# Kernel tuning notes

Hardware: AMD Instinct MI355X
Metric: run time of the kernel (lower is better)

The kernel has to match this reference:

```python
import jax, jax.numpy as jnp
import numpy as np

D_MODEL = 1024
N_HEADS = 16
HEAD_D = D_MODEL // N_HEADS  # 64


def setup_inputs() -> dict:
    key = jax.random.key(0)
    ks = jax.random.split(key, 10)
    s = 1.0 / np.sqrt(D_MODEL)
    x = jax.random.normal(ks[0], (4, 2048, D_MODEL), dtype=jnp.float32)
    # Per-head Q/K/V linears stacked along a head axis: W [H, d_model, d], b [H, d]
    Wq = jax.random.uniform(ks[1], (N_HEADS, D_MODEL, HEAD_D), jnp.float32, -s, s)
    bq = jax.random.uniform(ks[2], (N_HEADS, HEAD_D), jnp.float32, -s, s)
    Wk = jax.random.uniform(ks[3], (N_HEADS, D_MODEL, HEAD_D), jnp.float32, -s, s)
    bk = jax.random.uniform(ks[4], (N_HEADS, HEAD_D), jnp.float32, -s, s)
    Wv = jax.random.uniform(ks[5], (N_HEADS, D_MODEL, HEAD_D), jnp.float32, -s, s)
    bv = jax.random.uniform(ks[6], (N_HEADS, HEAD_D), jnp.float32, -s, s)
    Wo = jax.random.uniform(ks[7], (D_MODEL, D_MODEL), jnp.float32, -s, s)
    bo = jax.random.uniform(ks[8], (D_MODEL,), jnp.float32, -s, s)
    return {"x": x, "Wq": Wq, "bq": bq, "Wk": Wk, "bk": bk,
            "Wv": Wv, "bv": bv, "Wo": Wo, "bo": bo}


def reference(x, Wq, bq, Wk, bk, Wv, bv, Wo, bo):
    # x: [B, S, M]; per-head projections -> [B, H, S, d]
    Q = jnp.einsum('bsm,hmd->bhsd', x, Wq) + bq[None, :, None, :]
    K = jnp.einsum('bsm,hmd->bhsd', x, Wk) + bk[None, :, None, :]
    V = jnp.einsum('bsm,hmd->bhsd', x, Wv) + bv[None, :, None, :]
    scale = 1.0 / jnp.sqrt(jnp.asarray(HEAD_D, dtype=x.dtype))
    scores = jnp.einsum('bhqd,bhkd->bhqk', Q, K) * scale  # [B, H, S, S]
    attn = jax.nn.softmax(scores, axis=-1)
    out = jnp.einsum('bhqk,bhkd->bhqd', attn, V)  # [B, H, S, d]
    B, H, S, d = out.shape
    out = out.transpose(0, 2, 1, 3).reshape(B, S, H * d)  # concat heads
    # final projection (dropout is identity in eval mode)
    return out @ Wo.T + bo
```

## Files before the change

### kernel.cpp

```cpp
#include <hip/hip_runtime.h>
#include <stdint.h>

#define DEVI __device__ __forceinline__

typedef float f32x4 __attribute__((ext_vector_type(4)));
typedef float f32x16 __attribute__((ext_vector_type(16)));
typedef float float4v __attribute__((ext_vector_type(4)));
typedef short short8 __attribute__((ext_vector_type(8)));
typedef uint16_t u16x4 __attribute__((ext_vector_type(4)));
typedef uint32_t u32x4 __attribute__((ext_vector_type(4)));
typedef int i32x2 __attribute__((ext_vector_type(2)));

static constexpr float QSCALE = 0.125f * 1.44269504088896340736f;

DEVI uint16_t f2bf(float f) {
  uint32_t u = __builtin_bit_cast(uint32_t, f);
  return (uint16_t)((u + 0x7FFFu + ((u >> 16) & 1u)) >> 16);
}

DEVI void gload_lds16(const void* g, void* lds) {
  __builtin_amdgcn_global_load_lds(
      reinterpret_cast<const uint32_t __attribute__((address_space(1)))*>(
          reinterpret_cast<uintptr_t>(g)),
      reinterpret_cast<uint32_t __attribute__((address_space(3)))*>(
          reinterpret_cast<uintptr_t>(lds)),
      16, 0, 0);
}

DEVI short8 lds_frag(const uint16_t* tile, int row, int kByte) {
  return *(const short8*)((const char*)tile + row * 128 + (kByte ^ ((row & 7) << 4)));
}

DEVI f32x4 mfma16(short8 a, short8 b, f32x4 c) {
  return __builtin_amdgcn_mfma_f32_16x16x32_bf16(a, b, c, 0, 0, 0);
}
DEVI f32x16 mfma32(short8 a, short8 b, f32x16 c) {
  return __builtin_amdgcn_mfma_f32_32x32x16_bf16(a, b, c, 0, 0, 0);
}

DEVI uint32_t cvtpk(float lo, float hi) {
  uint32_t r;
  asm("v_cvt_pk_bf16_f32 %0, %1, %2" : "=v"(r) : "v"(lo), "v"(hi));
  return r;
}


__global__ void k_cvt_x(const float* __restrict__ x, uint16_t* __restrict__ xb) {
  const int i = blockIdx.x * blockDim.x + threadIdx.x;
  const float4v* p = (const float4v*)x + (size_t)i * 2;
  float4v a = p[0], b = p[1];
  alignas(16) uint16_t r[8];
  r[0] = f2bf(a[0]); r[1] = f2bf(a[1]); r[2] = f2bf(a[2]); r[3] = f2bf(a[3]);
  r[4] = f2bf(b[0]); r[5] = f2bf(b[1]); r[6] = f2bf(b[2]); r[7] = f2bf(b[3]);
  *((short8*)xb + i) = *(const short8*)r;
}

__global__ void k_cvt_wo(const float* __restrict__ Wo, uint16_t* __restrict__ Wob) {
  const int i = blockIdx.x * blockDim.x + threadIdx.x;
  const float4v* p = (const float4v*)Wo + (size_t)i * 2;
  float4v a = p[0], b = p[1];
  alignas(16) uint16_t r[8];
  r[0] = f2bf(a[0]); r[1] = f2bf(a[1]); r[2] = f2bf(a[2]); r[3] = f2bf(a[3]);
  r[4] = f2bf(b[0]); r[5] = f2bf(b[1]); r[6] = f2bf(b[2]); r[7] = f2bf(b[3]);
  *((short8*)Wob + i) = *(const short8*)r;
}

__global__ void k_cvt_wqkv(const float* __restrict__ Wq, const float* __restrict__ Wk,
                           const float* __restrict__ Wv, uint16_t* __restrict__ Wt) {
  __shared__ float tile[64][65];
  const int bx = blockIdx.x;
  const int sect = bx >> 8, h = (bx >> 4) & 15, kc = bx & 15;
  const float* W = sect == 0 ? Wq : (sect == 1 ? Wk : Wv);
  const float scal = sect == 0 ? QSCALE : 1.0f;
  const int t = threadIdx.x;
  const int r = t >> 2, cbase = (t & 3) * 16;
  const float* src = W + ((size_t)(h * 1024 + kc * 64 + r)) * 64 + cbase;
#pragma unroll
  for (int j = 0; j < 4; ++j) {
    float4v v = *(const float4v*)(src + j * 4);
    tile[r][cbase + j * 4 + 0] = v[0];
    tile[r][cbase + j * 4 + 1] = v[1];
    tile[r][cbase + j * 4 + 2] = v[2];
    tile[r][cbase + j * 4 + 3] = v[3];
  }
  __syncthreads();
  const int dd = t >> 2, kp = (t & 3) * 16;
  alignas(16) uint16_t tmp[16];
#pragma unroll
  for (int j = 0; j < 16; ++j) tmp[j] = f2bf(tile[kp + j][dd] * scal);
  const int n = sect * 1024 + h * 64 + dd;
  uint16_t* dst = Wt + (size_t)n * 1024 + kc * 64 + kp;
  *(short8*)dst = *(const short8*)tmp;
  *((short8*)dst + 1) = *(const short8*)(tmp + 8);
}

template <int MODE>
__global__ __launch_bounds__(256, 2) void gemm_k1024(
    const uint16_t* __restrict__ A, const uint16_t* __restrict__ Bt, int tiles_n,
    const float* __restrict__ bias_q, const float* __restrict__ bias_k,
    const float* __restrict__ bias_v,
    uint16_t* __restrict__ Qws, uint16_t* __restrict__ Kws, uint16_t* __restrict__ Vtws,
    float* __restrict__ outf) {
  __shared__ uint16_t As[2][128 * 64];
  __shared__ uint16_t Bs[2][128 * 64];

  const int tid = threadIdx.x, lane = tid & 63, wv = tid >> 6;
  const int m0 = (blockIdx.x / tiles_n) * 128;
  const int n0 = (blockIdx.x % tiles_n) * 128;
  const int wm = (wv >> 1) * 64, wn = (wv & 1) * 64;
  const int rin = lane >> 3;
  const int csw = ((lane & 7) ^ rin) * 16;

  const char* gA = (const char*)A;
  const char* gB = (const char*)Bt;

  f32x4 acc[4][4];
#pragma unroll
  for (int mi = 0; mi < 4; ++mi)
#pragma unroll
    for (int ni = 0; ni < 4; ++ni) acc[mi][ni] = (f32x4){0.f, 0.f, 0.f, 0.f};

  auto stage = [&](int buf, int kt) {
    const int k0b = kt * 128;
#pragma unroll
    for (int i = 0; i < 4; ++i) {
      const int rb = wv * 32 + i * 8;
      gload_lds16(gA + (size_t)(m0 + rb + rin) * 2048 + k0b + csw, &As[buf][rb * 64]);
      gload_lds16(gB + (size_t)(n0 + rb + rin) * 2048 + k0b + csw, &Bs[buf][rb * 64]);
    }
  };

  stage(0, 0);
  const int kb0 = (lane >> 4) * 16;
  for (int kt = 0; kt < 16; ++kt) {
    const int buf = kt & 1;
    __syncthreads();
    if (kt + 1 < 16) stage(buf ^ 1, kt + 1);
#pragma unroll
    for (int kk = 0; kk < 2; ++kk) {
      short8 af[4], bfr[4];
#pragma unroll
      for (int i = 0; i < 4; ++i) {
        af[i] = lds_frag(As[buf], wm + i * 16 + (lane & 15), kk * 64 + kb0);
        bfr[i] = lds_frag(Bs[buf], wn + i * 16 + (lane & 15), kk * 64 + kb0);
      }
#pragma unroll
      for (int mi = 0; mi < 4; ++mi)
#pragma unroll
        for (int ni = 0; ni < 4; ++ni) acc[mi][ni] = mfma16(af[mi], bfr[ni], acc[mi][ni]);
    }
  }

  const int col0 = n0 + wn + (lane & 15);
  const int row0 = m0 + wm + ((lane >> 4) << 2);
  if (MODE == 1) {
#pragma unroll
    for (int ni = 0; ni < 4; ++ni) {
      const int n = col0 + ni * 16;
      const float bv = bias_q[n];
#pragma unroll
      for (int mi = 0; mi < 4; ++mi) {
        const int mrow = row0 + mi * 16;
#pragma unroll
        for (int r = 0; r < 4; ++r)
          outf[(size_t)(mrow + r) * 1024 + n] = acc[mi][ni][r] + bv;
      }
    }
  } else {
#pragma unroll
    for (int ni = 0; ni < 4; ++ni) {
      const int n = col0 + ni * 16;
      const int sect = n >> 10, h = (n >> 6) & 15, dd = n & 63;
      float bv;
      if (sect == 0) bv = bias_q[h * 64 + dd] * QSCALE;
      else if (sect == 1) bv = bias_k[h * 64 + dd];
      else bv = bias_v[h * 64 + dd];
#pragma unroll
      for (int mi = 0; mi < 4; ++mi) {
        const int mrow = row0 + mi * 16;
        const int b = mrow >> 11, s = mrow & 2047;
        const int bh = b * 16 + h;
        if (sect == 2) {
          u16x4 pk;
#pragma unroll
          for (int r = 0; r < 4; ++r) pk[r] = f2bf(acc[mi][ni][r] + bv);
          *(u16x4*)(Vtws + ((size_t)bh * 64 + dd) * 2048 + s) = pk;
        } else {
          uint16_t* dst = (sect == 0 ? Qws : Kws) + ((size_t)bh * 2048 + s) * 64 + dd;
#pragma unroll
          for (int r = 0; r < 4; ++r) dst[(size_t)r * 64] = f2bf(acc[mi][ni][r] + bv);
        }
      }
    }
  }
}

__global__ __launch_bounds__(256, 2) void attn_fa(
    const uint16_t* __restrict__ Qws, const uint16_t* __restrict__ Kws,
    const uint16_t* __restrict__ Vtws, uint16_t* __restrict__ AttO) {
  __shared__ uint16_t Kl[2][64 * 64];
  __shared__ uint16_t Vl[2][64 * 64];

  const int tid = threadIdx.x, lane = tid & 63, wq = tid >> 6;
  const int bid = blockIdx.x;
  const int bh = (bid & 7) * 8 + (bid >> 7);
  const int q0 = ((bid >> 3) & 15) * 128;
  const int hi = lane >> 5;
  const int qc = lane & 31;

  const uint16_t* Qb = Qws + (size_t)bh * (2048 * 64);
  const uint16_t* Kb = Kws + (size_t)bh * (2048 * 64);
  const uint16_t* Vb = Vtws + (size_t)bh * (64 * 2048);

  const int lrow = lane >> 3;
  const int csw = ((lane & 7) ^ lrow) * 16;

  short8 qf[4];
  const int qrow = q0 + wq * 32 + qc;
#pragma unroll
  for (int c = 0; c < 4; ++c)
    qf[c] = *(const short8*)(Qb + (size_t)qrow * 64 + c * 16 + hi * 8);

  short8 ones;
#pragma unroll
  for (int j = 0; j < 8; ++j) ones[j] = (short)0x3F80;

  f32x16 o0 = {}, o1 = {};
  f32x16 accL = {};
  float m = 8.0f;

  auto stage = [&](int buf, int kt) {
    const int kv0 = kt * 64;
#pragma unroll
    for (int i = 0; i < 2; ++i) {
      const int rb = i * 32 + wq * 8;
      const int rt = rb + lrow;
      gload_lds16((const char*)Kb + (size_t)(kv0 + rt) * 128 + csw,
                  (char*)&Kl[buf][0] + rb * 128);
      gload_lds16((const char*)Vb + ((size_t)rt * 2048 + kv0) * 2 + csw,
                  (char*)&Vl[buf][0] + rb * 128);
    }
  };

  stage(0, 0);
  for (int kt = 0; kt < 32; ++kt) {
    const int buf = kt & 1;
    __syncthreads();
    if (kt + 1 < 32) stage(buf ^ 1, kt + 1);

    f32x16 p0 = {}, p1 = {};
    __builtin_amdgcn_s_setprio(1);
#pragma unroll
    for (int c = 0; c < 4; ++c) {
      short8 k0 = lds_frag(&Kl[buf][0], qc, c * 32 + hi * 16);
      short8 k1 = lds_frag(&Kl[buf][0], 32 + qc, c * 32 + hi * 16);
      p0 = mfma32(k0, qf[c], p0);
      p1 = mfma32(k1, qf[c], p1);
    }
    __builtin_amdgcn_s_setprio(0);

    float t8[8];
#pragma unroll
    for (int r = 0; r < 8; ++r)
      t8[r] = fmaxf(fmaxf(p0[2 * r], p0[2 * r + 1]),
                    fmaxf(p1[2 * r], p1[2 * r + 1]));
#pragma unroll
    for (int r = 0; r < 4; ++r) t8[r] = fmaxf(t8[r], t8[r + 4]);
    float mx = fmaxf(fmaxf(t8[0], t8[1]), fmaxf(t8[2], t8[3]));
    mx = fmaxf(mx, __shfl_xor(mx, 32, 64));
    if (__any(mx - m > 8.0f)) {
      const float nm = fmaxf(m, mx);
      const float al = __builtin_amdgcn_exp2f(m - nm);
      accL[0] *= al;
#pragma unroll
      for (int r = 0; r < 16; ++r) { o0[r] *= al; o1[r] *= al; }
      m = nm;
    }
#pragma unroll
    for (int r = 0; r < 16; ++r) p0[r] = __builtin_amdgcn_exp2f(p0[r] - m);
#pragma unroll
    for (int r = 0; r < 16; ++r) p1[r] = __builtin_amdgcn_exp2f(p1[r] - m);

    short8 pa[4];
#pragma unroll
    for (int km = 0; km < 2; ++km) {
#pragma unroll
      for (int bb = 0; bb < 2; ++bb) {
        const f32x16& p = km ? p1 : p0;
        uint32_t X0 = cvtpk(p[8 * bb + 0], p[8 * bb + 1]);
        uint32_t Y0 = cvtpk(p[8 * bb + 4], p[8 * bb + 5]);
        uint32_t X1 = cvtpk(p[8 * bb + 2], p[8 * bb + 3]);
        uint32_t Y1 = cvtpk(p[8 * bb + 6], p[8 * bb + 7]);
        i32x2 s0 = __builtin_amdgcn_permlane32_swap((int)X0, (int)Y0, false, false);
        i32x2 s1 = __builtin_amdgcn_permlane32_swap((int)X1, (int)Y1, false, false);
        u32x4 dw = {(uint32_t)s0[0], (uint32_t)s1[0], (uint32_t)s0[1], (uint32_t)s1[1]};
        pa[km * 2 + bb] = __builtin_bit_cast(short8, dw);
      }
    }

    __builtin_amdgcn_s_setprio(1);
#pragma unroll
    for (int ks = 0; ks < 4; ++ks) {
      short8 v0 = lds_frag(&Vl[buf][0], qc, ks * 32 + hi * 16);
      short8 v1 = lds_frag(&Vl[buf][0], 32 + qc, ks * 32 + hi * 16);
      o0 = mfma32(v0, pa[ks], o0);
      o1 = mfma32(v1, pa[ks], o1);
      accL = mfma32(ones, pa[ks], accL);
    }
    __builtin_amdgcn_s_setprio(0);
  }
  __syncthreads();

  const float inv = 1.0f / accL[0];
#pragma unroll
  for (int r = 0; r < 16; ++r) { o0[r] *= inv; o1[r] *= inv; }

  uint16_t* ep = (uint16_t*)Kl + wq * 2048;
#pragma unroll
  for (int no = 0; no < 2; ++no)
#pragma unroll
    for (int rg = 0; rg < 4; ++rg) {
      const f32x16& oo = no ? o1 : o0;
      const int d0 = no * 32 + rg * 8 + hi * 4;
      u16x4 pk;
#pragma unroll
      for (int j = 0; j < 4; ++j) pk[j] = f2bf(oo[rg * 4 + j]);
      *(u16x4*)((char*)ep + qc * 128 + ((d0 * 2) ^ ((qc & 7) << 4))) = pk;
    }
  const int b = bh >> 4, h = bh & 15;
#pragma unroll
  for (int it = 0; it < 4; ++it) {
    const int pos = it * 64 + lane;
    const int qq = pos >> 3, c = pos & 7;
    short8 vv = *(const short8*)((const char*)ep + qq * 128 + ((c * 16) ^ ((qq & 7) << 4)));
    *(short8*)(AttO + ((size_t)b * 2048 + q0 + wq * 32 + qq) * 1024 + h * 64 + c * 8) = vv;
  }
}


extern "C" void kernel_launch(void* const* d_in, const int* in_sizes, int n_in,
                              void* d_out, int out_size, void* d_ws, size_t ws_size,
                              hipStream_t stream) {
  (void)in_sizes; (void)n_in; (void)out_size; (void)ws_size;
  const float* x  = (const float*)d_in[0];
  const float* Wq = (const float*)d_in[1];
  const float* bq = (const float*)d_in[2];
  const float* Wk = (const float*)d_in[3];
  const float* bk = (const float*)d_in[4];
  const float* Wv = (const float*)d_in[5];
  const float* bv = (const float*)d_in[6];
  const float* Wo = (const float*)d_in[7];
  const float* bo = (const float*)d_in[8];
  float* out = (float*)d_out;

  char* ws = (char*)d_ws;
  uint16_t* Xb   = (uint16_t*)(ws);
  uint16_t* AttO = (uint16_t*)(ws);
  uint16_t* Wqkv = (uint16_t*)(ws + 16777216);
  uint16_t* Wob  = (uint16_t*)(ws + 23068672);
  uint16_t* Qws  = (uint16_t*)(ws + 25165824);
  uint16_t* Kws  = (uint16_t*)(ws + 41943040);
  uint16_t* Vt   = (uint16_t*)(ws + 58720256);

  k_cvt_x<<<4096, 256, 0, stream>>>(x, Xb);
  k_cvt_wqkv<<<768, 256, 0, stream>>>(Wq, Wk, Wv, Wqkv);
  k_cvt_wo<<<512, 256, 0, stream>>>(Wo, Wob);
  gemm_k1024<0><<<64 * 24, 256, 0, stream>>>(Xb, Wqkv, 24, bq, bk, bv, Qws, Kws, Vt, nullptr);
  attn_fa<<<1024, 256, 0, stream>>>(Qws, Kws, Vt, AttO);
  gemm_k1024<1><<<64 * 8, 256, 0, stream>>>(AttO, Wob, 8, bo, nullptr, nullptr,
                                            nullptr, nullptr, nullptr, out);
}
```

Measured before the change: 199.1 us.

## Process two query groups per wave in attention, compute row sums on VALU, swizzle GEMM blocks

Each attention wave now handles 64 query rows as two 32-row groups that share the same K/V LDS fragments. This halves the grid to 512 blocks and doubles K/V reuse per load. The softmax denominator is now a VALU sum with a cross-half shuffle instead of an extra MFMA against a ones vector. The GEMM kernels also remap block IDs with an XCD-style swizzle to improve L2 locality. In exchange, register pressure rises from the doubled accumulators, and with fewer blocks occupancy and wave-level parallelism may drop.

```diff
diff --git a/kernel.cpp b/kernel.cpp
--- a/kernel.cpp
+++ b/kernel.cpp
@@ -42,6 +42,35 @@
   uint32_t r;
   asm("v_cvt_pk_bf16_f32 %0, %1, %2" : "=v"(r) : "v"(lo), "v"(hi));
   return r;
+}
+
+DEVI void mk_pa(const f32x16& p0, const f32x16& p1, short8* pa) {
+#pragma unroll
+  for (int km = 0; km < 2; ++km) {
+#pragma unroll
+    for (int bb = 0; bb < 2; ++bb) {
+      const f32x16& p = km ? p1 : p0;
+      uint32_t X0 = cvtpk(p[8 * bb + 0], p[8 * bb + 1]);
+      uint32_t Y0 = cvtpk(p[8 * bb + 4], p[8 * bb + 5]);
+      uint32_t X1 = cvtpk(p[8 * bb + 2], p[8 * bb + 3]);
+      uint32_t Y1 = cvtpk(p[8 * bb + 6], p[8 * bb + 7]);
+      i32x2 s0 = __builtin_amdgcn_permlane32_swap((int)X0, (int)Y0, false, false);
+      i32x2 s1 = __builtin_amdgcn_permlane32_swap((int)X1, (int)Y1, false, false);
+      u32x4 dw = {(uint32_t)s0[0], (uint32_t)s1[0], (uint32_t)s0[1], (uint32_t)s1[1]};
+      pa[km * 2 + bb] = __builtin_bit_cast(short8, dw);
+    }
+  }
+}
+
+DEVI float tree_max(const f32x16& p0, const f32x16& p1) {
+  float t8[8];
+#pragma unroll
+  for (int r = 0; r < 8; ++r)
+    t8[r] = fmaxf(fmaxf(p0[2 * r], p0[2 * r + 1]),
+                  fmaxf(p1[2 * r], p1[2 * r + 1]));
+#pragma unroll
+  for (int r = 0; r < 4; ++r) t8[r] = fmaxf(t8[r], t8[r + 4]);
+  return fmaxf(fmaxf(t8[0], t8[1]), fmaxf(t8[2], t8[3]));
 }
 
 
@@ -105,8 +134,11 @@
   __shared__ uint16_t Bs[2][128 * 64];
 
   const int tid = threadIdx.x, lane = tid & 63, wv = tid >> 6;
-  const int m0 = (blockIdx.x / tiles_n) * 128;
-  const int n0 = (blockIdx.x % tiles_n) * 128;
+  const int cpx = (MODE == 0) ? 192 : 64;
+  const int bid = blockIdx.x;
+  const int swz = (bid & 7) * cpx + (bid >> 3);
+  const int m0 = (swz / tiles_n) * 128;
+  const int n0 = (swz % tiles_n) * 128;
   const int wm = (wv >> 1) * 64, wn = (wv & 1) * 64;
   const int rin = lane >> 3;
   const int csw = ((lane & 7) ^ rin) * 16;
@@ -198,13 +230,12 @@
 __global__ __launch_bounds__(256, 2) void attn_fa(
     const uint16_t* __restrict__ Qws, const uint16_t* __restrict__ Kws,
     const uint16_t* __restrict__ Vtws, uint16_t* __restrict__ AttO) {
-  __shared__ uint16_t Kl[2][64 * 64];
-  __shared__ uint16_t Vl[2][64 * 64];
+  __shared__ uint16_t SM[2][2][64 * 64];
 
   const int tid = threadIdx.x, lane = tid & 63, wq = tid >> 6;
   const int bid = blockIdx.x;
-  const int bh = (bid & 7) * 8 + (bid >> 7);
-  const int q0 = ((bid >> 3) & 15) * 128;
+  const int bh = (bid & 7) * 8 + (bid >> 6);
+  const int q0 = ((bid >> 3) & 7) * 256;
   const int hi = lane >> 5;
   const int qc = lane & 31;
 
@@ -215,19 +246,16 @@
   const int lrow = lane >> 3;
   const int csw = ((lane & 7) ^ lrow) * 16;
 
-  short8 qf[4];
-  const int qrow = q0 + wq * 32 + qc;
-#pragma unroll
-  for (int c = 0; c < 4; ++c)
-    qf[c] = *(const short8*)(Qb + (size_t)qrow * 64 + c * 16 + hi * 8);
-
-  short8 ones;
-#pragma unroll
-  for (int j = 0; j < 8; ++j) ones[j] = (short)0x3F80;
-
-  f32x16 o0 = {}, o1 = {};
-  f32x16 accL = {};
-  float m = 8.0f;
+  short8 qf[2][4];
+#pragma unroll
+  for (int g = 0; g < 2; ++g)
+#pragma unroll
+    for (int c = 0; c < 4; ++c)
+      qf[g][c] = *(const short8*)(Qb + (size_t)(q0 + wq * 64 + g * 32 + qc) * 64 +
+                                  c * 16 + hi * 8);
+
+  f32x16 oA0 = {}, oA1 = {}, oB0 = {}, oB1 = {};
+  float mA = 8.0f, mB = 8.0f, lA = 0.0f, lB = 0.0f;
 
   auto stage = [&](int buf, int kt) {
     const int kv0 = kt * 64;
@@ -236,9 +264,9 @@
       const int rb = i * 32 + wq * 8;
       const int rt = rb + lrow;
       gload_lds16((const char*)Kb + (size_t)(kv0 + rt) * 128 + csw,
-                  (char*)&Kl[buf][0] + rb * 128);
+                  (char*)&SM[buf][0][0] + rb * 128);
       gload_lds16((const char*)Vb + ((size_t)rt * 2048 + kv0) * 2 + csw,
-                  (char*)&Vl[buf][0] + rb * 128);
+                  (char*)&SM[buf][1][0] + rb * 128);
     }
   };
 
@@ -247,93 +275,117 @@
     const int buf = kt & 1;
     __syncthreads();
     if (kt + 1 < 32) stage(buf ^ 1, kt + 1);
-
-    f32x16 p0 = {}, p1 = {};
+    const uint16_t* Kl = &SM[buf][0][0];
+    const uint16_t* Vl = &SM[buf][1][0];
+
+    f32x16 pA0 = {}, pA1 = {}, pB0 = {}, pB1 = {};
     __builtin_amdgcn_s_setprio(1);
 #pragma unroll
     for (int c = 0; c < 4; ++c) {
-      short8 k0 = lds_frag(&Kl[buf][0], qc, c * 32 + hi * 16);
-      short8 k1 = lds_frag(&Kl[buf][0], 32 + qc, c * 32 + hi * 16);
-      p0 = mfma32(k0, qf[c], p0);
-      p1 = mfma32(k1, qf[c], p1);
+      short8 k0 = lds_frag(Kl, qc, c * 32 + hi * 16);
+      short8 k1 = lds_frag(Kl, 32 + qc, c * 32 + hi * 16);
+      pA0 = mfma32(k0, qf[0][c], pA0);
+      pA1 = mfma32(k1, qf[0][c], pA1);
+      pB0 = mfma32(k0, qf[1][c], pB0);
+      pB1 = mfma32(k1, qf[1][c], pB1);
     }
     __builtin_amdgcn_s_setprio(0);
 
-    float t8[8];
-#pragma unroll
-    for (int r = 0; r < 8; ++r)
-      t8[r] = fmaxf(fmaxf(p0[2 * r], p0[2 * r + 1]),
-                    fmaxf(p1[2 * r], p1[2 * r + 1]));
-#pragma unroll
-    for (int r = 0; r < 4; ++r) t8[r] = fmaxf(t8[r], t8[r + 4]);
-    float mx = fmaxf(fmaxf(t8[0], t8[1]), fmaxf(t8[2], t8[3]));
-    mx = fmaxf(mx, __shfl_xor(mx, 32, 64));
-    if (__any(mx - m > 8.0f)) {
-      const float nm = fmaxf(m, mx);
-      const float al = __builtin_amdgcn_exp2f(m - nm);
-      accL[0] *= al;
-#pragma unroll
-      for (int r = 0; r < 16; ++r) { o0[r] *= al; o1[r] *= al; }
-      m = nm;
-    }
-#pragma unroll
-    for (int r = 0; r < 16; ++r) p0[r] = __builtin_amdgcn_exp2f(p0[r] - m);
-#pragma unroll
-    for (int r = 0; r < 16; ++r) p1[r] = __builtin_amdgcn_exp2f(p1[r] - m);
-
-    short8 pa[4];
-#pragma unroll
-    for (int km = 0; km < 2; ++km) {
-#pragma unroll
-      for (int bb = 0; bb < 2; ++bb) {
-        const f32x16& p = km ? p1 : p0;
-        uint32_t X0 = cvtpk(p[8 * bb + 0], p[8 * bb + 1]);
-        uint32_t Y0 = cvtpk(p[8 * bb + 4], p[8 * bb + 5]);
-        uint32_t X1 = cvtpk(p[8 * bb + 2], p[8 * bb + 3]);
-        uint32_t Y1 = cvtpk(p[8 * bb + 6], p[8 * bb + 7]);
-        i32x2 s0 = __builtin_amdgcn_permlane32_swap((int)X0, (int)Y0, false, false);
-        i32x2 s1 = __builtin_amdgcn_permlane32_swap((int)X1, (int)Y1, false, false);
-        u32x4 dw = {(uint32_t)s0[0], (uint32_t)s1[0], (uint32_t)s0[1], (uint32_t)s1[1]};
-        pa[km * 2 + bb] = __builtin_bit_cast(short8, dw);
+    float mxA = tree_max(pA0, pA1);
+    float mxB = tree_max(pB0, pB1);
+    mxA = fmaxf(mxA, __shfl_xor(mxA, 32, 64));
+    mxB = fmaxf(mxB, __shfl_xor(mxB, 32, 64));
+    if (__any(fmaxf(mxA - mA, mxB - mB) > 8.0f)) {
+      const float nmA = fmaxf(mA, mxA), nmB = fmaxf(mB, mxB);
+      const float alA = __builtin_amdgcn_exp2f(mA - nmA);
+      const float alB = __builtin_amdgcn_exp2f(mB - nmB);
+      lA *= alA; lB *= alB;
+#pragma unroll
+      for (int r = 0; r < 16; ++r) {
+        oA0[r] *= alA; oA1[r] *= alA;
+        oB0[r] *= alB; oB1[r] *= alB;
       }
+      mA = nmA; mB = nmB;
+    }
+    short8 paA[4], paB[4];
+    {
+#pragma unroll
+      for (int r = 0; r < 16; ++r) pA0[r] = __builtin_amdgcn_exp2f(pA0[r] - mA);
+#pragma unroll
+      for (int r = 0; r < 16; ++r) pA1[r] = __builtin_amdgcn_exp2f(pA1[r] - mA);
+      float s[16];
+#pragma unroll
+      for (int r = 0; r < 16; ++r) s[r] = pA0[r] + pA1[r];
+#pragma unroll
+      for (int r = 0; r < 8; ++r) s[r] += s[r + 8];
+#pragma unroll
+      for (int r = 0; r < 4; ++r) s[r] += s[r + 4];
+      float sum = (s[0] + s[1]) + (s[2] + s[3]);
+      sum += __shfl_xor(sum, 32, 64);
+      lA += sum;
+      mk_pa(pA0, pA1, paA);
+    }
+    {
+#pragma unroll
+      for (int r = 0; r < 16; ++r) pB0[r] = __builtin_amdgcn_exp2f(pB0[r] - mB);
+#pragma unroll
+      for (int r = 0; r < 16; ++r) pB1[r] = __builtin_amdgcn_exp2f(pB1[r] - mB);
+      float s[16];
+#pragma unroll
+      for (int r = 0; r < 16; ++r) s[r] = pB0[r] + pB1[r];
+#pragma unroll
+      for (int r = 0; r < 8; ++r) s[r] += s[r + 8];
+#pragma unroll
+      for (int r = 0; r < 4; ++r) s[r] += s[r + 4];
+      float sum = (s[0] + s[1]) + (s[2] + s[3]);
+      sum += __shfl_xor(sum, 32, 64);
+      lB += sum;
+      mk_pa(pB0, pB1, paB);
     }
 
     __builtin_amdgcn_s_setprio(1);
 #pragma unroll
     for (int ks = 0; ks < 4; ++ks) {
-      short8 v0 = lds_frag(&Vl[buf][0], qc, ks * 32 + hi * 16);
-      short8 v1 = lds_frag(&Vl[buf][0], 32 + qc, ks * 32 + hi * 16);
-      o0 = mfma32(v0, pa[ks], o0);
-      o1 = mfma32(v1, pa[ks], o1);
-      accL = mfma32(ones, pa[ks], accL);
+      short8 v0 = lds_frag(Vl, qc, ks * 32 + hi * 16);
+      short8 v1 = lds_frag(Vl, 32 + qc, ks * 32 + hi * 16);
+      oA0 = mfma32(v0, paA[ks], oA0);
+      oA1 = mfma32(v1, paA[ks], oA1);
+      oB0 = mfma32(v0, paB[ks], oB0);
+      oB1 = mfma32(v1, paB[ks], oB1);
     }
     __builtin_amdgcn_s_setprio(0);
   }
   __syncthreads();
 
-  const float inv = 1.0f / accL[0];
-#pragma unroll
-  for (int r = 0; r < 16; ++r) { o0[r] *= inv; o1[r] *= inv; }
-
-  uint16_t* ep = (uint16_t*)Kl + wq * 2048;
-#pragma unroll
-  for (int no = 0; no < 2; ++no)
-#pragma unroll
-    for (int rg = 0; rg < 4; ++rg) {
-      const f32x16& oo = no ? o1 : o0;
-      const int d0 = no * 32 + rg * 8 + hi * 4;
-      u16x4 pk;
-#pragma unroll
-      for (int j = 0; j < 4; ++j) pk[j] = f2bf(oo[rg * 4 + j]);
-      *(u16x4*)((char*)ep + qc * 128 + ((d0 * 2) ^ ((qc & 7) << 4))) = pk;
-    }
+  const float invA = 1.0f / lA, invB = 1.0f / lB;
+#pragma unroll
+  for (int r = 0; r < 16; ++r) {
+    oA0[r] *= invA; oA1[r] *= invA;
+    oB0[r] *= invB; oB1[r] *= invB;
+  }
+
+  char* ep = (char*)&SM[0][0][0] + wq * 8192;
+#pragma unroll
+  for (int g = 0; g < 2; ++g)
+#pragma unroll
+    for (int no = 0; no < 2; ++no)
+#pragma unroll
+      for (int rg = 0; rg < 4; ++rg) {
+        const f32x16& oo = g ? (no ? oB1 : oB0) : (no ? oA1 : oA0);
+        const int row = g * 32 + qc;
+        const int d0 = no * 32 + rg * 8 + hi * 4;
+        u16x4 pk;
+#pragma unroll
+        for (int j = 0; j < 4; ++j) pk[j] = f2bf(oo[rg * 4 + j]);
+        *(u16x4*)(ep + row * 128 + ((d0 * 2) ^ ((row & 7) << 4))) = pk;
+      }
   const int b = bh >> 4, h = bh & 15;
 #pragma unroll
-  for (int it = 0; it < 4; ++it) {
+  for (int it = 0; it < 8; ++it) {
     const int pos = it * 64 + lane;
     const int qq = pos >> 3, c = pos & 7;
-    short8 vv = *(const short8*)((const char*)ep + qq * 128 + ((c * 16) ^ ((qq & 7) << 4)));
-    *(short8*)(AttO + ((size_t)b * 2048 + q0 + wq * 32 + qq) * 1024 + h * 64 + c * 8) = vv;
+    short8 vv = *(const short8*)(ep + qq * 128 + ((c * 16) ^ ((qq & 7) << 4)));
+    *(short8*)(AttO + ((size_t)b * 2048 + q0 + wq * 64 + qq) * 1024 + h * 64 + c * 8) = vv;
   }
 }
 
@@ -366,7 +418,7 @@
   k_cvt_wqkv<<<768, 256, 0, stream>>>(Wq, Wk, Wv, Wqkv);
   k_cvt_wo<<<512, 256, 0, stream>>>(Wo, Wob);
   gemm_k1024<0><<<64 * 24, 256, 0, stream>>>(Xb, Wqkv, 24, bq, bk, bv, Qws, Kws, Vt, nullptr);
-  attn_fa<<<1024, 256, 0, stream>>>(Qws, Kws, Vt, AttO);
+  attn_fa<<<512, 256, 0, stream>>>(Qws, Kws, Vt, AttO);
   gemm_k1024<1><<<64 * 8, 256, 0, stream>>>(AttO, Wob, 8, bo, nullptr, nullptr,
                                             nullptr, nullptr, nullptr, out);
 }
```

New measurement: 190.4 us. -4.4%, faster.
